# Performance work log

Measured on AMD Instinct MI355X. Metric: run time of the kernel, lower is better.

The kernel has to match this reference:

```python
import jax, jax.numpy as jnp
import numpy as np

B, T, D, E, P = 32, 8192, 256, 16, 64  # batch, tokens, dim, num_spectral_blocks, pixels_per_patch


def setup_inputs() -> dict:
    key = jax.random.key(0)
    k1, k2, k3, k4 = jax.random.split(key, 4)
    x = jax.random.normal(k1, (B, T, D), dtype=jnp.float32)
    block_indices = jax.random.randint(k2, (B, T), 0, E)
    # per-expert Linear(dim -> pixels_per_patch): weight [E, D, P], bias [E, P]
    W = jax.random.normal(k3, (E, D, P), dtype=jnp.float32) * 0.02
    b = jax.random.normal(k4, (E, P), dtype=jnp.float32) * 0.02
    return {"x": x, "W": W, "b": b, "block_indices": block_indices}


def reference(x, W, b, block_indices):
    # Each token [b, t] is routed to expert block_indices[b, t]; that expert's
    # Linear(dim -> pixels_per_patch) produces the output row. Loop is over the
    # small fixed expert count (16), fully vectorized over tokens.
    num_experts = W.shape[0]
    out = jnp.zeros(x.shape[:2] + (W.shape[2],), dtype=x.dtype)
    for e in range(num_experts):
        y = x @ W[e] + b[e]                       # [B, T, P]
        sel = (block_indices == e)[..., None]      # [B, T, 1]
        out = jnp.where(sel, y, out)
    return out
```

## Files before the change

kernel.cpp:

```cpp
#include <hip/hip_runtime.h>

#define NT (32 * 8192)
#define DIM 256
#define NE 16
#define NP 64
#define NCH 64
#define CAPC 352

typedef short bf16x8 __attribute__((ext_vector_type(8)));
typedef float f32x4 __attribute__((ext_vector_type(4)));
typedef int i32x4 __attribute__((ext_vector_type(4)));

__device__ __forceinline__ unsigned short f2bf(float f) {
  unsigned int u = __builtin_bit_cast(unsigned int, f);
  u += 0x7fffu + ((u >> 16) & 1u);
  return (unsigned short)(u >> 16);
}

__global__ void k_prep(const float* __restrict__ W, const int* __restrict__ idx,
                       unsigned short* __restrict__ Wt, int* __restrict__ cnt_ec,
                       int* __restrict__ bucket) {
  int t = threadIdx.x;
  if (blockIdx.x >= 64) {
    int gid = (blockIdx.x - 64) * 256 + t;
    int e = gid >> 10;
    int n = (gid >> 4) & 63;
    int k0 = (gid & 15) << 4;
    const float* src = W + e * (DIM * NP) + n;
    unsigned short* dst = Wt + ((e * NP + n) * DIM + k0);
    #pragma unroll
    for (int j = 0; j < 16; ++j) dst[j] = f2bf(src[(k0 + j) * NP]);
    return;
  }
  __shared__ int cur[NE];
  if (t < NE) cur[t] = 0;
  __syncthreads();
  int c = blockIdx.x;
  int b0 = c * 4096;
  #pragma unroll
  for (int i = 0; i < 16; ++i) {
    int tok = b0 + i * 256 + t;
    int e = idx[tok];
    int pos = atomicAdd(&cur[e], 1);
    if (pos < CAPC) bucket[(e * NCH + c) * CAPC + pos] = tok;
  }
  __syncthreads();
  if (t < NE) cnt_ec[t * NCH + c] = cur[t] < CAPC ? cur[t] : CAPC;
}

__global__ __launch_bounds__(256, 4) void k_gemm(
    const float* __restrict__ x, const unsigned short* __restrict__ Wt,
    const float* __restrict__ bvec, const int* __restrict__ cnt_ec,
    const int* __restrict__ bucket, float* __restrict__ out) {
  int e = blockIdx.x >> 6;
  int slice = blockIdx.x & 63;
  int tid = threadIdx.x;
  int w = tid >> 6;
  int lane = tid & 63;
  int cc = lane & 15, q = lane >> 4;

  __shared__ __align__(16) unsigned short wlds[NP * DIM];

  const unsigned short* wb = Wt + e * NP * DIM;
  #pragma unroll
  for (int it = 0; it < 8; ++it) {
    int lin = (it * 256 + tid) * 16;
    i32x4 v = *(const i32x4*)((const char*)wb + lin);
    int sw = lin ^ (((lin >> 9) & 7) << 4);
    *(i32x4*)((char*)wlds + sw) = v;
  }

  float bias[4];
  #pragma unroll
  for (int nf = 0; nf < 4; ++nf) bias[nf] = bvec[e * NP + nf * 16 + cc];

  int base0[4], swz[4];
  #pragma unroll
  for (int nf = 0; nf < 4; ++nf) {
    int n = nf * 16 + cc;
    base0[nf] = (n << 9) + (q << 4);
    swz[nf] = (n & 7) << 4;
  }

  __syncthreads();

  int s = slice * 4 + w;
  int c = s >> 2;
  int sub = s & 3;

  int rows_ec = cnt_ec[e * NCH + c];
  int ntiles = (rows_ec + 15) >> 4;
  const int* bkt = bucket + (e * NCH + c) * CAPC;

  for (int rt = sub; rt < ntiles; rt += 4) {
    int r0 = rt << 4;
    int rows = rows_ec - r0;
    if (rows > 16) rows = 16;

    int myr = cc < rows ? cc : 0;
    int tok = bkt[r0 + myr];
    const float* xr = x + (long)tok * DIM + q * 8;

    f32x4 va[16];
    #pragma unroll
    for (int ks = 0; ks < 8; ++ks) {
      va[2 * ks]     = *(const f32x4*)(xr + ks * 32);
      va[2 * ks + 1] = *(const f32x4*)(xr + ks * 32 + 4);
    }

    f32x4 acc[4];
    #pragma unroll
    for (int nf = 0; nf < 4; ++nf)
      acc[nf] = (f32x4){bias[nf], bias[nf], bias[nf], bias[nf]};

    #pragma unroll
    for (int ks = 0; ks < 8; ++ks) {
      bf16x8 a;
      #pragma unroll
      for (int j = 0; j < 4; ++j) {
        a[j]     = (short)f2bf(va[2 * ks][j]);
        a[4 + j] = (short)f2bf(va[2 * ks + 1][j]);
      }
      #pragma unroll
      for (int nf = 0; nf < 4; ++nf) {
        const bf16x8 bf = *(const bf16x8*)(
            (const char*)wlds + ((base0[nf] + (ks << 6)) ^ swz[nf]));
        acc[nf] = __builtin_amdgcn_mfma_f32_16x16x32_bf16(a, bf, acc[nf], 0, 0, 0);
      }
    }

    #pragma unroll
    for (int r = 0; r < 4; ++r) {
      int m = q * 4 + r;
      if (m < rows) {
        int tk = bkt[r0 + m];
        float* orow = out + (long)tk * NP + cc;
        #pragma unroll
        for (int nf = 0; nf < 4; ++nf) orow[nf * 16] = acc[nf][r];
      }
    }
  }
}

extern "C" void kernel_launch(void* const* d_in, const int* in_sizes, int n_in,
                              void* d_out, int out_size, void* d_ws, size_t ws_size,
                              hipStream_t stream) {
  const float* x = (const float*)d_in[0];
  const float* W = (const float*)d_in[1];
  const float* b = (const float*)d_in[2];
  const int* idx = (const int*)d_in[3];
  float* out = (float*)d_out;

  int* ws = (int*)d_ws;
  int* cnt_ec = ws;
  int* bucket = ws + 1024;
  unsigned short* Wt = (unsigned short*)(ws + 1024 + NE * NCH * CAPC);

  k_prep<<<128, 256, 0, stream>>>(W, idx, Wt, cnt_ec, bucket);
  k_gemm<<<NE * 64, 256, 0, stream>>>(x, Wt, b, cnt_ec, bucket, out);
}
```

Baseline: 452.1 us.

## Double-buffer gathered x rows across tiles and vectorize output stores

Rewrites the per-wave tile loop as a ping-pong pipeline. The next tile's x rows and output token indices are loaded into a second register buffer while the current tile is converted and run through MFMA, with sched_barrier keeping the loads issued early. Output columns are remapped so each lane owns 4 contiguous columns, which lets each row be written with one 16-byte store instead of four strided scalar stores, and the bias is loaded as one vector. Launch bounds drop from 4 to 2 blocks per SM to make room for the doubled register buffers, which lowers occupancy.

```diff
diff --git a/kernel.cpp b/kernel.cpp
--- a/kernel.cpp
+++ b/kernel.cpp
@@ -48,7 +48,63 @@
   if (t < NE) cnt_ec[t * NCH + c] = cur[t] < CAPC ? cur[t] : CAPC;
 }
 
-__global__ __launch_bounds__(256, 4) void k_gemm(
+
+#define BURST(VA, TOK)                                                    \
+  do {                                                                    \
+    const float* xr_ = x + (long)(TOK) * DIM + q * 8;                     \
+    _Pragma("unroll")                                                     \
+    for (int ks = 0; ks < 8; ++ks) {                                      \
+      VA[2 * ks]     = *(const f32x4*)(xr_ + ks * 32);                    \
+      VA[2 * ks + 1] = *(const f32x4*)(xr_ + ks * 32 + 4);                \
+    }                                                                     \
+  } while (0)
+
+#define GTOK(RT) ({ int r0_ = (RT) << 4; int rows_ = rows_ec - r0_;       \
+                    if (rows_ > 16) rows_ = 16;                           \
+                    bkt[r0_ + (cc < rows_ ? cc : 0)]; })
+
+#define LOAD_STK(DST, RT)                                                 \
+  do { int r0_ = (RT) << 4; int rows_ = rows_ec - r0_;                    \
+       if (rows_ > 16) rows_ = 16;                                        \
+       _Pragma("unroll")                                                  \
+       for (int r = 0; r < 4; ++r) {                                      \
+         int m = q * 4 + r; DST[r] = bkt[m < rows_ ? r0_ + m : r0_];      \
+       } } while (0)
+
+#define TILE_COMPUTE_STORE(VA, STK, RT)                                   \
+  do {                                                                    \
+    int r0_ = (RT) << 4;                                                  \
+    int rows_ = rows_ec - r0_; if (rows_ > 16) rows_ = 16;                \
+    f32x4 acc[4];                                                         \
+    _Pragma("unroll")                                                     \
+    for (int nf = 0; nf < 4; ++nf)                                        \
+      acc[nf] = (f32x4){bias4[nf], bias4[nf], bias4[nf], bias4[nf]};      \
+    _Pragma("unroll")                                                     \
+    for (int ks = 0; ks < 8; ++ks) {                                      \
+      bf16x8 a;                                                           \
+      _Pragma("unroll")                                                   \
+      for (int j = 0; j < 4; ++j) {                                       \
+        a[j]     = (short)f2bf(VA[2 * ks][j]);                            \
+        a[4 + j] = (short)f2bf(VA[2 * ks + 1][j]);                        \
+      }                                                                   \
+      _Pragma("unroll")                                                   \
+      for (int nf = 0; nf < 4; ++nf) {                                    \
+        const bf16x8 bf = *(const bf16x8*)(                               \
+            (const char*)wlds + ((base0[nf] + (ks << 6)) ^ swz[nf]));     \
+        acc[nf] = __builtin_amdgcn_mfma_f32_16x16x32_bf16(a, bf, acc[nf], 0, 0, 0); \
+      }                                                                   \
+    }                                                                     \
+    _Pragma("unroll")                                                     \
+    for (int r = 0; r < 4; ++r) {                                         \
+      int m = q * 4 + r;                                                  \
+      if (m < rows_) {                                                    \
+        f32x4 v = {acc[0][r], acc[1][r], acc[2][r], acc[3][r]};           \
+        *(f32x4*)(out + (long)STK[r] * NP + 4 * cc) = v;                  \
+      }                                                                   \
+    }                                                                     \
+  } while (0)
+
+__global__ __launch_bounds__(256, 2) void k_gemm(
     const float* __restrict__ x, const unsigned short* __restrict__ Wt,
     const float* __restrict__ bvec, const int* __restrict__ cnt_ec,
     const int* __restrict__ bucket, float* __restrict__ out) {
@@ -70,14 +126,12 @@
     *(i32x4*)((char*)wlds + sw) = v;
   }
 
-  float bias[4];
-  #pragma unroll
-  for (int nf = 0; nf < 4; ++nf) bias[nf] = bvec[e * NP + nf * 16 + cc];
+  f32x4 bias4 = *(const f32x4*)(bvec + e * NP + 4 * cc);
 
   int base0[4], swz[4];
   #pragma unroll
   for (int nf = 0; nf < 4; ++nf) {
-    int n = nf * 16 + cc;
+    int n = 4 * cc + nf;
     base0[nf] = (n << 9) + (q << 4);
     swz[nf] = (n & 7) << 4;
   }
@@ -92,53 +146,35 @@
   int ntiles = (rows_ec + 15) >> 4;
   const int* bkt = bucket + (e * NCH + c) * CAPC;
 
-  for (int rt = sub; rt < ntiles; rt += 4) {
-    int r0 = rt << 4;
-    int rows = rows_ec - r0;
-    if (rows > 16) rows = 16;
+  if (sub >= ntiles) return;
 
-    int myr = cc < rows ? cc : 0;
-    int tok = bkt[r0 + myr];
-    const float* xr = x + (long)tok * DIM + q * 8;
+  f32x4 vaA[16], vaB[16];
+  int stkA[4], stkB[4];
+  int rt = sub;
 
-    f32x4 va[16];
-    #pragma unroll
-    for (int ks = 0; ks < 8; ++ks) {
-      va[2 * ks]     = *(const f32x4*)(xr + ks * 32);
-      va[2 * ks + 1] = *(const f32x4*)(xr + ks * 32 + 4);
-    }
+  int tokA = GTOK(rt);
+  BURST(vaA, tokA);
+  LOAD_STK(stkA, rt);
+  int tok_next = (rt + 4 < ntiles) ? GTOK(rt + 4) : 0;
 
-    f32x4 acc[4];
-    #pragma unroll
-    for (int nf = 0; nf < 4; ++nf)
-      acc[nf] = (f32x4){bias[nf], bias[nf], bias[nf], bias[nf]};
+  for (;;) {
+    bool haveN = (rt + 4) < ntiles;
+    if (haveN) { BURST(vaB, tok_next); LOAD_STK(stkB, rt + 4); }
+    int tok_n2 = (rt + 8 < ntiles) ? GTOK(rt + 8) : 0;
+    __builtin_amdgcn_sched_barrier(0);
+    TILE_COMPUTE_STORE(vaA, stkA, rt);
+    rt += 4;
+    if (!haveN) break;
+    tok_next = tok_n2;
 
-    #pragma unroll
-    for (int ks = 0; ks < 8; ++ks) {
-      bf16x8 a;
-      #pragma unroll
-      for (int j = 0; j < 4; ++j) {
-        a[j]     = (short)f2bf(va[2 * ks][j]);
-        a[4 + j] = (short)f2bf(va[2 * ks + 1][j]);
-      }
-      #pragma unroll
-      for (int nf = 0; nf < 4; ++nf) {
-        const bf16x8 bf = *(const bf16x8*)(
-            (const char*)wlds + ((base0[nf] + (ks << 6)) ^ swz[nf]));
-        acc[nf] = __builtin_amdgcn_mfma_f32_16x16x32_bf16(a, bf, acc[nf], 0, 0, 0);
-      }
-    }
-
-    #pragma unroll
-    for (int r = 0; r < 4; ++r) {
-      int m = q * 4 + r;
-      if (m < rows) {
-        int tk = bkt[r0 + m];
-        float* orow = out + (long)tk * NP + cc;
-        #pragma unroll
-        for (int nf = 0; nf < 4; ++nf) orow[nf * 16] = acc[nf][r];
-      }
-    }
+    haveN = (rt + 4) < ntiles;
+    if (haveN) { BURST(vaA, tok_next); LOAD_STK(stkA, rt + 4); }
+    tok_n2 = (rt + 8 < ntiles) ? GTOK(rt + 8) : 0;
+    __builtin_amdgcn_sched_barrier(0);
+    TILE_COMPUTE_STORE(vaB, stkB, rt);
+    rt += 4;
+    if (!haveN) break;
+    tok_next = tok_n2;
   }
 }
 
```

After: 401.2 us. -11.3%, faster.
